# Performance work log

Measured on AMD Instinct MI355X. Metric: run time of the kernel, lower is better.

The kernel has to match this reference:

```python
import jax, jax.numpy as jnp
import numpy as np

B, T, D, N, K, H = 2, 2048, 2048, 16, 8, 128
WIN = 1024                      # sliding_window_size
SOFT_CAP = 50.0                 # attn_logits_soft_cap
SCALAR = 0.08838834764831845    # query_pre_attn_scalar = head_dim**-0.5
K_MASK = -2.3819763e+38
ROPE_BASE = 10000.0
ROPE_SCALE = 1.0


def apply_rope(x, positions):
    # x: [B, T, heads, H]; positions: [B, T]
    head_dim = x.shape[-1]
    half = head_dim // 2
    timescale = ROPE_BASE ** (2.0 * jnp.arange(half, dtype=jnp.float32) / head_dim)
    sinusoid = positions[..., None].astype(jnp.float32) / timescale / ROPE_SCALE  # [B,T,half]
    sin = jnp.sin(sinusoid)[:, :, None, :]
    cos = jnp.cos(sinusoid)[:, :, None, :]
    first, second = jnp.split(x, 2, axis=-1)
    return jnp.concatenate(
        [first * cos - second * sin, second * cos + first * sin], axis=-1
    ).astype(x.dtype)


def setup_inputs() -> dict:
    key = jax.random.key(0)
    k0, k1, k2, k3 = jax.random.split(key, 4)
    x = jax.random.normal(k0, (B, T, D), jnp.float32)
    wq = jax.random.normal(k1, (N, D, H), jnp.float32) * (D ** -0.5)
    wkv = jax.random.normal(k2, (2, K, D, H), jnp.float32) * (D ** -0.5)
    wo = jax.random.normal(k3, (N, H, D), jnp.float32) * ((N * H) ** -0.5)
    segment_pos = jnp.broadcast_to(jnp.arange(T, dtype=jnp.int32), (B, T))
    attn_mask = jnp.broadcast_to(jnp.tril(jnp.ones((T, T), dtype=bool)), (B, T, T))  # causal
    return {"x": x, "wq": wq, "wkv": wkv, "wo": wo,
            "segment_pos": segment_pos, "attn_mask": attn_mask}


def reference(x, wq, wkv, wo, segment_pos, attn_mask):
    # --- projections ---
    q = jnp.einsum('BTD,NDH->BTNH', x, wq)          # [B,T,N,H]
    kv = jnp.einsum('BTD,CKDH->CBTKH', x, wkv)      # [2,B,T,K,H]
    k_proj, v_proj = kv[0], kv[1]
    # --- RoPE + query scaling ---
    q = apply_rope(q, segment_pos) * SCALAR
    k_proj = apply_rope(k_proj, segment_pos)
    # --- GQA logits ---
    G = N // K
    qg = q.reshape(B, T, K, G, H)
    logits = jnp.einsum('BTKGH,BSKH->BTKGS', qg, k_proj).reshape(B, T, N, T)
    # --- soft cap ---
    logits = jnp.tanh(logits / SOFT_CAP) * SOFT_CAP
    # --- sliding-window mask combined with causal attn_mask ---
    all_ones = jnp.ones(attn_mask.shape, dtype=attn_mask.dtype)
    sliding_mask = jnp.triu(all_ones, -WIN + 1) * jnp.tril(all_ones, WIN - 1)
    mask = sliding_mask * attn_mask                  # [B,T,S]
    padded_logits = jnp.where(mask[:, :, None, :], logits, K_MASK)
    probs = jax.nn.softmax(padded_logits, axis=-1).astype(k_proj.dtype)
    # --- GQA weighted values ---
    encoded = jnp.einsum('BTKGS,BSKH->BTKGH',
                         probs.reshape(B, T, K, G, T), v_proj).reshape(B, T, N, H)
    # --- output projection ---
    return jnp.einsum('BTNH,NHD->BTD', encoded, wo)
```

## Files before the change

### kernel.cpp

```cpp
#include <hip/hip_runtime.h>
#include <stdint.h>

#define BDIM 2
#define TDIM 2048
#define DDIM 2048
#define NHEADS 16
#define KVH 8
#define HDIM 128
#define WINSZ 1024
#define BT (BDIM*TDIM)
#define NHD (NHEADS*HDIM)
#define QKVC 4096

typedef unsigned short u16;
typedef __attribute__((ext_vector_type(8))) short bf16x8;
typedef __attribute__((ext_vector_type(4))) float f32x4;

__device__ __forceinline__ u16 f2bf(float f) {
  union { float f; unsigned u; } v; v.f = f;
  unsigned r = v.u + 0x7FFFu + ((v.u >> 16) & 1u);
  return (u16)(r >> 16);
}
__device__ __forceinline__ float bf2f(u16 u) {
  union { unsigned u; float f; } v; v.u = ((unsigned)u) << 16;
  return v.f;
}

__device__ __forceinline__ void gl_lds16(const u16* g, u16* l) {
  __builtin_amdgcn_global_load_lds((const __attribute__((address_space(1))) void*)g,
                                   (__attribute__((address_space(3))) void*)l, 16, 0, 0);
}

__global__ void k_rope_table(const int* __restrict__ seg, float2* __restrict__ tab) {
  int t = blockIdx.x, b = blockIdx.y, i = threadIdx.x;
  int pos = seg[b*TDIM + t];
  float inv_ts = exp2f(-(float)i * (13.287712379549449f/64.0f));
  float ang = (float)pos * inv_ts;
  tab[(size_t)(b*TDIM + t)*64 + i] = make_float2(cosf(ang), sinf(ang));
}

__global__ void k_cvt_bf16(const float* __restrict__ x, u16* __restrict__ y, int n4) {
  int i = blockIdx.x*blockDim.x + threadIdx.x;
  if (i < n4) {
    float4 v = ((const float4*)x)[i];
    ushort4 o;
    o.x = f2bf(v.x); o.y = f2bf(v.y); o.z = f2bf(v.z); o.w = f2bf(v.w);
    ((ushort4*)y)[i] = o;
  }
}

template<int MODE>
__global__ void k_build_wt(const float* __restrict__ s0p, const float* __restrict__ s1p,
                           u16* __restrict__ dst) {
  __shared__ float tl[32][33];
  int tx = threadIdx.x, ty = threadIdx.y;
  int r0 = blockIdx.x*32, c0 = blockIdx.y*32;
  #pragma unroll
  for (int i = 0; i < 4; i++) {
    int r = r0 + tx, c = c0 + ty + i*8;
    const float* sp; size_t off;
    if (MODE == 0) {
      if (r < 2048) { sp = s0p; off = (size_t)(r >> 7)*262144u + (size_t)(r & 127); }
      else { int j = r - 2048; sp = s1p; off = (size_t)((j >> 10)*8 + ((j >> 7) & 7))*262144u + (size_t)(j & 127); }
      off += (size_t)c * 128u;
    } else {
      sp = s0p; off = (size_t)c * 2048u + (size_t)r;
    }
    tl[tx][ty + i*8] = sp[off];
  }
  __syncthreads();
  #pragma unroll
  for (int i = 0; i < 4; i++) {
    int rl = ty + i*8;
    dst[(size_t)(r0 + rl)*2048u + (size_t)(c0 + tx)] = f2bf(tl[rl][tx]);
  }
}

template<int F32OUT>
__global__ __launch_bounds__(256) void k_gemm(const u16* __restrict__ A, const u16* __restrict__ Bt,
                                              void* __restrict__ Cout, int M, int Ncols, int Kdim, int ldc) {
  __shared__ u16 As[128*64];
  __shared__ u16 Bs[128*64];
  const int tid = threadIdx.x, lane = tid & 63, wave = tid >> 6;
  const int m0 = blockIdx.x * 128, n0 = blockIdx.y * 128;
  const int wr = wave >> 1, wc = wave & 1;
  const int l15 = lane & 15, lg = lane >> 4;
  f32x4 acc[4][4] = {};
  for (int kt = 0; kt < Kdim; kt += 64) {
    __syncthreads();
    #pragma unroll
    for (int i = 0; i < 4; i++) {
      int chb = i*256 + wave*64;
      int ch = chb + lane;
      int r = ch >> 3, cc = ch & 7;
      gl_lds16(A + (size_t)(m0 + r)*Kdim + kt + cc*8, As + chb*8);
      gl_lds16(Bt + (size_t)(n0 + r)*Kdim + kt + cc*8, Bs + chb*8);
    }
    __syncthreads();
    #pragma unroll
    for (int ks = 0; ks < 2; ks++) {
      bf16x8 af[4], bf[4];
      int kk = ks*32 + lg*8;
      #pragma unroll
      for (int mt = 0; mt < 4; mt++) af[mt] = *(const bf16x8*)(As + (wr*64 + mt*16 + l15)*64 + kk);
      #pragma unroll
      for (int nt = 0; nt < 4; nt++) bf[nt] = *(const bf16x8*)(Bs + (wc*64 + nt*16 + l15)*64 + kk);
      #pragma unroll
      for (int mt = 0; mt < 4; mt++)
        #pragma unroll
        for (int nt = 0; nt < 4; nt++)
          acc[mt][nt] = __builtin_amdgcn_mfma_f32_16x16x32_bf16(af[mt], bf[nt], acc[mt][nt], 0, 0, 0);
    }
  }
  #pragma unroll
  for (int mt = 0; mt < 4; mt++) {
    int row = m0 + wr*64 + mt*16 + lg*4;
    #pragma unroll
    for (int nt = 0; nt < 4; nt++) {
      int col = n0 + wc*64 + nt*16 + l15;
      #pragma unroll
      for (int j = 0; j < 4; j++) {
        if (F32OUT) ((float*)Cout)[(size_t)(row + j)*ldc + col] = acc[mt][nt][j];
        else        ((u16*)Cout)[(size_t)(row + j)*ldc + col] = f2bf(acc[mt][nt][j]);
      }
    }
  }
}

template<int F32OUT>
__global__ __launch_bounds__(512, 2) void k_gemm8(const u16* __restrict__ A, const u16* __restrict__ Bt,
                                                  void* __restrict__ Cout, int M, int Ncols, int Kdim, int ldc) {
  __shared__ u16 As[2][256*64];
  __shared__ u16 Bs[2][256*64];
  const int tid = threadIdx.x, lane = tid & 63, wave = tid >> 6;
  const int l15 = lane & 15, lg = lane >> 4;
  const int wm = wave >> 2, wn = wave & 3;
  const int gx = M >> 8, gy = Ncols >> 8;
  const int nwg = gx * gy;
  int bid = blockIdx.x;
  int q = nwg >> 3, r = nwg & 7;
  int xcd = bid & 7, idx = bid >> 3;
  int wg = (xcd < r ? xcd*(q+1) : r*(q+1) + (xcd - r)*q) + idx;
  const int m0 = (wg % gx) * 256, n0 = (wg / gx) * 256;

  const int st_r = tid >> 3;
  const int st_c = (tid & 7) ^ (st_r & 7);

  const u16* Ag = A + (size_t)(m0 + st_r)*Kdim + st_c*8;
  const u16* Bg = Bt + (size_t)(n0 + st_r)*Kdim + st_c*8;

  auto stage = [&](int t, int h) {
    int buf = t & 1;
    if (h < 2) {
      const u16* g = Bg + (size_t)(h*128)*Kdim + t*64;
      u16* d = &Bs[buf][h*8192 + wave*512];
      gl_lds16(g, d);
      gl_lds16(g + (size_t)64*Kdim, d + 4096);
    } else {
      int hh = h - 2;
      const u16* g = Ag + (size_t)(hh*128)*Kdim + t*64;
      u16* d = &As[buf][hh*8192 + wave*512];
      gl_lds16(g, d);
      gl_lds16(g + (size_t)64*Kdim, d + 4096);
    }
  };

  const int aBase = (wm*128 + l15) * 128;
  const int bBase = (wn*64 + l15) * 128;
  const int kx0 = ((lg) ^ (l15 & 7)) << 4;
  const int kx1 = ((4 + lg) ^ (l15 & 7)) << 4;

  f32x4 acc[8][4] = {};
  bf16x8 af[4][2], bfr[4][2];

  stage(0,0); stage(0,1); stage(0,2); stage(0,3);
  asm volatile("s_waitcnt vmcnt(4)" ::: "memory");
  stage(1,0); stage(1,1); stage(1,2);
  asm volatile("s_waitcnt vmcnt(6)" ::: "memory");
  __builtin_amdgcn_s_barrier();

  const int NT = Kdim >> 6;

#define MFMA_Q(MS, NS)                                                          \
  { _Pragma("unroll") for (int mf = 0; mf < 4; mf++)                            \
    _Pragma("unroll") for (int nf = 0; nf < 2; nf++) {                          \
      acc[(MS)+mf][(NS)+nf] = __builtin_amdgcn_mfma_f32_16x16x32_bf16(af[mf][0], bfr[(NS)+nf][0], acc[(MS)+mf][(NS)+nf], 0, 0, 0); \
      acc[(MS)+mf][(NS)+nf] = __builtin_amdgcn_mfma_f32_16x16x32_bf16(af[mf][1], bfr[(NS)+nf][1], acc[(MS)+mf][(NS)+nf], 0, 0, 0); \
  } }

  for (int t = 0; t < NT; ++t) {
    const int cur = t & 1;
    const char* Ab = (const char*)&As[cur][0];
    const char* Bb = (const char*)&Bs[cur][0];
    #pragma unroll
    for (int mf = 0; mf < 4; mf++) {
      af[mf][0] = *(const bf16x8*)(Ab + aBase + mf*2048 + kx0);
      af[mf][1] = *(const bf16x8*)(Ab + aBase + mf*2048 + kx1);
    }
    #pragma unroll
    for (int nf = 0; nf < 2; nf++) {
      bfr[nf][0] = *(const bf16x8*)(Bb + bBase + nf*2048 + kx0);
      bfr[nf][1] = *(const bf16x8*)(Bb + bBase + nf*2048 + kx1);
    }
    if (t + 1 < NT) stage(t+1, 3);
    asm volatile("s_waitcnt lgkmcnt(8)" ::: "memory");
    __builtin_amdgcn_s_barrier();
    asm volatile("" ::: "memory");
    __builtin_amdgcn_s_setprio(1);
    MFMA_Q(0, 0)
    __builtin_amdgcn_s_setprio(0);
    __builtin_amdgcn_s_barrier();
    #pragma unroll
    for (int nf = 2; nf < 4; nf++) {
      bfr[nf][0] = *(const bf16x8*)(Bb + bBase + nf*2048 + kx0);
      bfr[nf][1] = *(const bf16x8*)(Bb + bBase + nf*2048 + kx1);
    }
    __builtin_amdgcn_s_barrier();
    asm volatile("" ::: "memory");
    __builtin_amdgcn_s_setprio(1);
    MFMA_Q(0, 2)
    __builtin_amdgcn_s_setprio(0);
    __builtin_amdgcn_s_barrier();
    #pragma unroll
    for (int mf = 0; mf < 4; mf++) {
      af[mf][0] = *(const bf16x8*)(Ab + aBase + 8192 + mf*2048 + kx0);
      af[mf][1] = *(const bf16x8*)(Ab + aBase + 8192 + mf*2048 + kx1);
    }
    if (t + 2 < NT) { stage(t+2, 0); stage(t+2, 1); }
    __builtin_amdgcn_s_barrier();
    asm volatile("" ::: "memory");
    __builtin_amdgcn_s_setprio(1);
    MFMA_Q(4, 2)
    __builtin_amdgcn_s_setprio(0);
    __builtin_amdgcn_s_barrier();
    if (t + 2 < NT) {
      stage(t+2, 2);
      asm volatile("s_waitcnt vmcnt(6)" ::: "memory");
    } else if (t + 1 < NT) {
      asm volatile("s_waitcnt vmcnt(0)" ::: "memory");
    }
    __builtin_amdgcn_s_barrier();
    asm volatile("" ::: "memory");
    __builtin_amdgcn_s_setprio(1);
    MFMA_Q(4, 0)
    __builtin_amdgcn_s_setprio(0);
    __builtin_amdgcn_s_barrier();
  }
#undef MFMA_Q

  #pragma unroll
  for (int mf = 0; mf < 8; mf++) {
    int row = m0 + wm*128 + mf*16 + lg*4;
    #pragma unroll
    for (int nf = 0; nf < 4; nf++) {
      int col = n0 + wn*64 + nf*16 + l15;
      #pragma unroll
      for (int j = 0; j < 4; j++) {
        if (F32OUT) ((float*)Cout)[(size_t)(row + j)*ldc + col] = acc[mf][nf][j];
        else        ((u16*)Cout)[(size_t)(row + j)*ldc + col] = f2bf(acc[mf][nf][j]);
      }
    }
  }
}

__global__ void k_rope2(u16* __restrict__ qkv, const float2* __restrict__ tab) {
  const int tid = threadIdx.x;
  const int bt = blockIdx.x;
  const int h = tid >> 3, g = tid & 7;
  const int col0 = (h < 16 ? h*128 : 2048 + (h - 16)*128) + g*8;
  const float sc = (h < 16) ? 0.08838834764831845f : 1.0f;
  u16* row = qkv + (size_t)bt*QKVC;
  bf16x8 v1 = *(const bf16x8*)(row + col0);
  bf16x8 v2 = *(const bf16x8*)(row + col0 + 64);
  const float4* t4 = (const float4*)(tab + (size_t)bt*64 + g*8);
  bf16x8 r1, r2;
  #pragma unroll
  for (int i = 0; i < 4; i++) {
    float4 cs2 = t4[i];
    float f0 = bf2f((u16)v1[2*i]),   s0 = bf2f((u16)v2[2*i]);
    float f1 = bf2f((u16)v1[2*i+1]), s1 = bf2f((u16)v2[2*i+1]);
    r1[2*i]   = (short)f2bf((f0*cs2.x - s0*cs2.y)*sc);
    r2[2*i]   = (short)f2bf((s0*cs2.x + f0*cs2.y)*sc);
    r1[2*i+1] = (short)f2bf((f1*cs2.z - s1*cs2.w)*sc);
    r2[2*i+1] = (short)f2bf((s1*cs2.z + f1*cs2.w)*sc);
  }
  *(bf16x8*)(row + col0) = r1;
  *(bf16x8*)(row + col0 + 64) = r2;
}

__global__ void k_build_vt(const u16* __restrict__ qkv, u16* __restrict__ vT) {
  __shared__ u16 tl[32][33];
  int tx = threadIdx.x, ty = threadIdx.y;
  int t0 = blockIdx.x*32, h0 = blockIdx.y*32, bk = blockIdx.z;
  const u16* src = qkv + (size_t)(bk >> 3)*TDIM*QKVC + 3072 + (bk & 7)*HDIM;
  #pragma unroll
  for (int i = 0; i < 4; i++)
    tl[ty + i*8][tx] = src[(size_t)(t0 + ty + i*8)*QKVC + h0 + tx];
  __syncthreads();
  u16* dst = vT + (size_t)bk*HDIM*TDIM;
  #pragma unroll
  for (int i = 0; i < 4; i++)
    dst[(size_t)(h0 + ty + i*8)*TDIM + t0 + tx] = tl[tx][ty + i*8];
}

__device__ __forceinline__ void stage_tiles(const u16* __restrict__ kg, const u16* __restrict__ vg,
                                            u16* ldsK, u16* ldsV, int tid) {
  const int w = tid >> 6;
  const int rK = tid >> 4, cK = tid & 15;
  u16* dK = ldsK + w*512;
  gl_lds16(kg + (size_t)rK*QKVC + ((cK ^ (rK & 15)) << 3), dK);
  gl_lds16(kg + (size_t)(rK + 32)*QKVC + ((cK ^ ((rK + 32) & 15)) << 3), dK + 4096);
  const int rV = tid >> 3, cV = tid & 7;
  u16* dV = ldsV + w*512;
  gl_lds16(vg + (size_t)rV*TDIM + ((cV ^ (rV & 7)) << 3), dV);
  gl_lds16(vg + (size_t)(rV + 64)*TDIM + ((cV ^ ((rV + 64) & 7)) << 3), dV + 4096);
}

__global__ __launch_bounds__(512, 4) void k_attn(const u16* __restrict__ qkv, const u16* __restrict__ vT,
                                                 u16* __restrict__ enc) {
  __shared__ u16 Kb[2][64*128];
  __shared__ u16 Vb[2][128*64];
  __shared__ u16 Pl[8][16*64];
  const int tid = threadIdx.x;
  const int lane = tid & 63, wave = tid >> 6;
  const int l15 = lane & 15, lg = lane >> 4;
  const int wg = blockIdx.x;
  const int lin = (wg & 7)*64 + (wg >> 3);
  const int qt = lin & 31, kvh = (lin >> 5) & 7, b = lin >> 8;
  const int n = kvh*2 + (wave >> 2);
  const int t0 = qt * 64;
  const int lo_row = t0 + (wave & 3)*16, hi_row = lo_row + 15;

  bf16x8 qf[4];
  {
    const u16* qb = qkv + (size_t)(b*TDIM + lo_row + l15)*QKVC + n*HDIM + lg*8;
    #pragma unroll
    for (int ks = 0; ks < 4; ks++) qf[ks] = *(const bf16x8*)(qb + ks*32);
  }
  f32x4 o[8] = {};
  f32x4 o_l = {};
  const short one_bf = (short)0x3F80;
  const bf16x8 ones = {one_bf, one_bf, one_bf, one_bf, one_bf, one_bf, one_bf, one_bf};

  const u16* kgb = qkv + (size_t)(b*TDIM)*QKVC + 2048 + kvh*HDIM;
  const u16* vgb = vT + (size_t)(b*KVH + kvh)*HDIM*TDIM;

  const float L0 = 1.4426950408889634f;
  const float L1 = -1.9235933878519513e-4f;
  const float L2 = 3.0777094205631089e-8f;
  const float BIAS = -72.13475204444817f;

  const int s_begin = (t0 >= 1024) ? (t0 - 1024) : 0;
  stage_tiles(kgb + (size_t)s_begin*QKVC, vgb + s_begin, Kb[0], Vb[0], tid);
  int cur = 0;
  for (int s0 = s_begin; s0 <= t0; s0 += 64) {
    if (s0 + 64 <= t0) {
      stage_tiles(kgb + (size_t)(s0 + 64)*QKVC, vgb + (s0 + 64), Kb[cur ^ 1], Vb[cur ^ 1], tid);
      asm volatile("s_waitcnt vmcnt(4)" ::: "memory");
    } else {
      asm volatile("s_waitcnt vmcnt(0)" ::: "memory");
    }
    __builtin_amdgcn_s_barrier();
    __builtin_amdgcn_sched_barrier(0);

    const u16* Kc = Kb[cur];
    const u16* Vc = Vb[cur];
    f32x4 sc4[4];
    #pragma unroll
    for (int c = 0; c < 4; c++) {
      const int cLo = s0 + c*16;
      bool anyLive = (cLo <= hi_row) && (cLo + 15 >= lo_row - (WINSZ - 1));
      bool full    = (cLo + 15 <= lo_row) && (cLo >= hi_row - (WINSZ - 1));
      f32x4 a = {0.f, 0.f, 0.f, 0.f};
      if (anyLive) {
        int krow = c*16 + l15;
        __builtin_amdgcn_s_setprio(1);
        #pragma unroll
        for (int ks = 0; ks < 4; ks++) {
          bf16x8 kf = *(const bf16x8*)(Kc + krow*128 + (((ks*4 + lg) ^ l15) << 3));
          a = __builtin_amdgcn_mfma_f32_16x16x32_bf16(qf[ks], kf, a, 0, 0, 0);
        }
        __builtin_amdgcn_s_setprio(0);
        if (full) {
          #pragma unroll
          for (int j = 0; j < 4; j++) {
            float z = a[j];
            float u = z*z;
            float tt = __builtin_fmaf(u, __builtin_fmaf(u, L2, L1), L0);
            a[j] = exp2f(__builtin_fmaf(z, tt, BIAS));
          }
        } else {
          #pragma unroll
          for (int j = 0; j < 4; j++) {
            int scol = cLo + l15;
            int trow = lo_row + lg*4 + j;
            float z = a[j];
            float u = z*z;
            float tt = __builtin_fmaf(u, __builtin_fmaf(u, L2, L1), L0);
            float p = exp2f(__builtin_fmaf(z, tt, BIAS));
            bool ok = (scol <= trow) && (scol >= trow - (WINSZ - 1));
            a[j] = ok ? p : 0.f;
          }
        }
      }
      sc4[c] = a;
    }
    #pragma unroll
    for (int c = 0; c < 4; c++)
      #pragma unroll
      for (int j = 0; j < 4; j++) {
        int prow = lg*4 + j, pcol = c*16 + l15;
        int off = prow*128 + pcol*2; off ^= (prow & 7) << 4;
        *(u16*)((char*)(&Pl[wave][0]) + off) = f2bf(sc4[c][j]);
      }
    __builtin_amdgcn_s_setprio(1);
    #pragma unroll
    for (int ks = 0; ks < 2; ks++) {
      int roff = l15*128 + ks*64 + lg*16; roff ^= (l15 & 7) << 4;
      bf16x8 pf = *(const bf16x8*)((char*)(&Pl[wave][0]) + roff);
      o_l = __builtin_amdgcn_mfma_f32_16x16x32_bf16(pf, ones, o_l, 0, 0, 0);
      #pragma unroll
      for (int ct = 0; ct < 8; ct++) {
        int vrow = ct*16 + l15;
        bf16x8 vf = *(const bf16x8*)(Vc + vrow*64 + (((ks*4 + lg) ^ (l15 & 7)) << 3));
        o[ct] = __builtin_amdgcn_mfma_f32_16x16x32_bf16(pf, vf, o[ct], 0, 0, 0);
      }
    }
    __builtin_amdgcn_s_setprio(0);
    __builtin_amdgcn_s_barrier();
    cur ^= 1;
  }
  #pragma unroll
  for (int j = 0; j < 4; j++) {
    float inv = __fdividef(1.f, o_l[j]);
    int row = lo_row + lg*4 + j;
    u16* eb = enc + (size_t)(b*TDIM + row)*NHD + n*HDIM;
    #pragma unroll
    for (int ct = 0; ct < 8; ct++)
      eb[ct*16 + l15] = f2bf(o[ct][j] * inv);
  }
}

extern "C" void kernel_launch(void* const* d_in, const int* in_sizes, int n_in,
                              void* d_out, int out_size, void* d_ws, size_t ws_size,
                              hipStream_t stream) {
  const float* x   = (const float*)d_in[0];
  const float* wq  = (const float*)d_in[1];
  const float* wkv = (const float*)d_in[2];
  const float* wo  = (const float*)d_in[3];
  const int*   seg = (const int*)d_in[4];
  float* out = (float*)d_out;

  char* ws = (char*)d_ws;
  u16*    x_bf   = (u16*)(ws);
  u16*    wt_qkv = (u16*)(ws + (16u << 20));
  u16*    qkv    = (u16*)(ws + (32u << 20));
  u16*    vT     = (u16*)(ws + (64u << 20));
  u16*    enc    = (u16*)(ws + (72u << 20));
  u16*    wo_t   = (u16*)(ws + (88u << 20));
  float2* tab    = (float2*)(ws + (96u << 20));

  k_rope_table<<<dim3(TDIM, BDIM), 64, 0, stream>>>(seg, tab);
  k_cvt_bf16<<<(BT*DDIM/4 + 255)/256, 256, 0, stream>>>(x, x_bf, BT*DDIM/4);
  k_build_wt<0><<<dim3(128, 64), dim3(32, 8), 0, stream>>>(wq, wkv, wt_qkv);
  k_build_wt<1><<<dim3(64, 64), dim3(32, 8), 0, stream>>>(wo, nullptr, wo_t);
  k_gemm8<0><<<dim3((BT/256)*(QKVC/256)), 512, 0, stream>>>(x_bf, wt_qkv, qkv, BT, QKVC, DDIM, QKVC);
  k_rope2<<<dim3(BT), 192, 0, stream>>>(qkv, tab);
  k_build_vt<<<dim3(TDIM/32, HDIM/32, BDIM*KVH), dim3(32, 8), 0, stream>>>(qkv, vT);
  k_attn<<<dim3(512), 512, 0, stream>>>(qkv, vT, enc);
  k_gemm<1><<<dim3(BT/128, DDIM/128), 256, 0, stream>>>(enc, wo_t, out, BT, DDIM, NHD, DDIM);
}
```

Before: 216.9 us.

## Software-pipeline attention loop: overlap next-tile QK with current PV, cheaper tanh poly

```diff
diff --git a/kernel.cpp b/kernel.cpp
--- a/kernel.cpp
+++ b/kernel.cpp
@@ -303,19 +303,6 @@
     dst[(size_t)(h0 + ty + i*8)*TDIM + t0 + tx] = tl[tx][ty + i*8];
 }
 
-__device__ __forceinline__ void stage_tiles(const u16* __restrict__ kg, const u16* __restrict__ vg,
-                                            u16* ldsK, u16* ldsV, int tid) {
-  const int w = tid >> 6;
-  const int rK = tid >> 4, cK = tid & 15;
-  u16* dK = ldsK + w*512;
-  gl_lds16(kg + (size_t)rK*QKVC + ((cK ^ (rK & 15)) << 3), dK);
-  gl_lds16(kg + (size_t)(rK + 32)*QKVC + ((cK ^ ((rK + 32) & 15)) << 3), dK + 4096);
-  const int rV = tid >> 3, cV = tid & 7;
-  u16* dV = ldsV + w*512;
-  gl_lds16(vg + (size_t)rV*TDIM + ((cV ^ (rV & 7)) << 3), dV);
-  gl_lds16(vg + (size_t)(rV + 64)*TDIM + ((cV ^ ((rV + 64) & 7)) << 3), dV + 4096);
-}
-
 __global__ __launch_bounds__(512, 4) void k_attn(const u16* __restrict__ qkv, const u16* __restrict__ vT,
                                                  u16* __restrict__ enc) {
   __shared__ u16 Kb[2][64*128];
@@ -346,47 +333,55 @@
   const u16* vgb = vT + (size_t)(b*KVH + kvh)*HDIM*TDIM;
 
   const float L0 = 1.4426950408889634f;
-  const float L1 = -1.9235933878519513e-4f;
-  const float L2 = 3.0777094205631089e-8f;
+  const float C1L = -1.9235933878519513e-4f;
   const float BIAS = -72.13475204444817f;
 
-  const int s_begin = (t0 >= 1024) ? (t0 - 1024) : 0;
-  stage_tiles(kgb + (size_t)s_begin*QKVC, vgb + s_begin, Kb[0], Vb[0], tid);
-  int cur = 0;
-  for (int s0 = s_begin; s0 <= t0; s0 += 64) {
-    if (s0 + 64 <= t0) {
-      stage_tiles(kgb + (size_t)(s0 + 64)*QKVC, vgb + (s0 + 64), Kb[cur ^ 1], Vb[cur ^ 1], tid);
-      asm volatile("s_waitcnt vmcnt(4)" ::: "memory");
-    } else {
-      asm volatile("s_waitcnt vmcnt(0)" ::: "memory");
-    }
-    __builtin_amdgcn_s_barrier();
-    __builtin_amdgcn_sched_barrier(0);
-
-    const u16* Kc = Kb[cur];
-    const u16* Vc = Vb[cur];
-    f32x4 sc4[4];
+  const int rK = tid >> 4, cK = tid & 15;
+  const int rV = tid >> 3, cV = tid & 7;
+  auto stageK = [&](int s, u16* Kbb) {
+    const u16* kg = kgb + (size_t)s*QKVC;
+    u16* dK = Kbb + wave*512;
+    gl_lds16(kg + (size_t)rK*QKVC + ((cK ^ (rK & 15)) << 3), dK);
+    gl_lds16(kg + (size_t)(rK + 32)*QKVC + ((cK ^ ((rK + 32) & 15)) << 3), dK + 4096);
+  };
+  auto stageV = [&](int s, u16* Vbb) {
+    const u16* vg = vgb + s;
+    u16* dV = Vbb + wave*512;
+    gl_lds16(vg + (size_t)rV*TDIM + ((cV ^ (rV & 7)) << 3), dV);
+    gl_lds16(vg + (size_t)(rV + 64)*TDIM + ((cV ^ ((rV + 64) & 7)) << 3), dV + 4096);
+  };
+
+  f32x4 nsc[4];
+  auto qk_raw = [&](int s0t, const u16* Kc) {
     #pragma unroll
     for (int c = 0; c < 4; c++) {
-      const int cLo = s0 + c*16;
+      const int cLo = s0t + c*16;
       bool anyLive = (cLo <= hi_row) && (cLo + 15 >= lo_row - (WINSZ - 1));
-      bool full    = (cLo + 15 <= lo_row) && (cLo >= hi_row - (WINSZ - 1));
       f32x4 a = {0.f, 0.f, 0.f, 0.f};
       if (anyLive) {
         int krow = c*16 + l15;
-        __builtin_amdgcn_s_setprio(1);
         #pragma unroll
         for (int ks = 0; ks < 4; ks++) {
           bf16x8 kf = *(const bf16x8*)(Kc + krow*128 + (((ks*4 + lg) ^ l15) << 3));
           a = __builtin_amdgcn_mfma_f32_16x16x32_bf16(qf[ks], kf, a, 0, 0, 0);
         }
-        __builtin_amdgcn_s_setprio(0);
+      }
+      nsc[c] = a;
+    }
+  };
+  auto sm_write = [&](int s0t) {
+    #pragma unroll
+    for (int c = 0; c < 4; c++) {
+      const int cLo = s0t + c*16;
+      bool anyLive = (cLo <= hi_row) && (cLo + 15 >= lo_row - (WINSZ - 1));
+      bool full    = (cLo + 15 <= lo_row) && (cLo >= hi_row - (WINSZ - 1));
+      f32x4 a = nsc[c];
+      if (anyLive) {
         if (full) {
           #pragma unroll
           for (int j = 0; j < 4; j++) {
             float z = a[j];
-            float u = z*z;
-            float tt = __builtin_fmaf(u, __builtin_fmaf(u, L2, L1), L0);
+            float tt = __builtin_fmaf(z*z, C1L, L0);
             a[j] = exp2f(__builtin_fmaf(z, tt, BIAS));
           }
         } else {
@@ -395,25 +390,22 @@
             int scol = cLo + l15;
             int trow = lo_row + lg*4 + j;
             float z = a[j];
-            float u = z*z;
-            float tt = __builtin_fmaf(u, __builtin_fmaf(u, L2, L1), L0);
+            float tt = __builtin_fmaf(z*z, C1L, L0);
             float p = exp2f(__builtin_fmaf(z, tt, BIAS));
             bool ok = (scol <= trow) && (scol >= trow - (WINSZ - 1));
             a[j] = ok ? p : 0.f;
           }
         }
       }
-      sc4[c] = a;
-    }
-    #pragma unroll
-    for (int c = 0; c < 4; c++)
       #pragma unroll
       for (int j = 0; j < 4; j++) {
         int prow = lg*4 + j, pcol = c*16 + l15;
         int off = prow*128 + pcol*2; off ^= (prow & 7) << 4;
-        *(u16*)((char*)(&Pl[wave][0]) + off) = f2bf(sc4[c][j]);
-      }
-    __builtin_amdgcn_s_setprio(1);
+        *(u16*)((char*)(&Pl[wave][0]) + off) = f2bf(a[j]);
+      }
+    }
+  };
+  auto pv = [&](const u16* Vc) {
     #pragma unroll
     for (int ks = 0; ks < 2; ks++) {
       int roff = l15*128 + ks*64 + lg*16; roff ^= (l15 & 7) << 4;
@@ -426,9 +418,40 @@
         o[ct] = __builtin_amdgcn_mfma_f32_16x16x32_bf16(pf, vf, o[ct], 0, 0, 0);
       }
     }
+  };
+
+  const int s_begin = (t0 >= 1024) ? (t0 - 1024) : 0;
+  stageK(s_begin, Kb[0]);
+  stageV(s_begin, Vb[0]);
+  if (s_begin + 64 <= t0) {
+    stageK(s_begin + 64, Kb[1]);
+    asm volatile("s_waitcnt vmcnt(4)" ::: "memory");
+  } else {
+    asm volatile("s_waitcnt vmcnt(2)" ::: "memory");
+  }
+  __builtin_amdgcn_s_barrier();
+  __builtin_amdgcn_sched_barrier(0);
+  qk_raw(s_begin, Kb[0]);
+  sm_write(s_begin);
+
+  int ic = 0;
+  for (int s0 = s_begin; s0 <= t0; s0 += 64, ic ^= 1) {
+    const int sn = s0 + 64;
+    const bool hn = (sn <= t0), hn2 = (sn + 64 <= t0);
+    if (hn)  stageV(sn, Vb[ic ^ 1]);
+    if (hn2) stageK(sn + 64, Kb[ic]);
+    if (hn2)      { asm volatile("s_waitcnt vmcnt(4)" ::: "memory"); }
+    else if (hn)  { asm volatile("s_waitcnt vmcnt(2)" ::: "memory"); }
+    else          { asm volatile("s_waitcnt vmcnt(0)" ::: "memory"); }
+    __builtin_amdgcn_s_barrier();
+    __builtin_amdgcn_sched_barrier(0);
+    __builtin_amdgcn_s_setprio(1);
+    if (hn) qk_raw(sn, Kb[ic ^ 1]);
+    pv(Vb[ic]);
     __builtin_amdgcn_s_setprio(0);
-    __builtin_amdgcn_s_barrier();
-    cur ^= 1;
+    if (hn) sm_write(sn);
+    __builtin_amdgcn_sched_barrier(0);
+    __builtin_amdgcn_s_barrier();
   }
   #pragma unroll
   for (int j = 0; j < 4; j++) {
```

New measurement: 242.5 us. +11.8%, slower.
